# Kernel optimization log

Measured on AMD Instinct MI355X. Metric: run time of the kernel, lower is better.

The kernel has to match this reference:

```python
import jax, jax.numpy as jnp
import numpy as np

D_MODEL = 1024
NUM_ATOMS = 16384
TEMPERATURE = 1.0
NEG_INF = -1e9


def setup_inputs() -> dict:
    key = jax.random.key(0)
    kx, kd, km = jax.random.split(key, 3)
    x = jax.random.normal(kx, (4, 2048, D_MODEL), dtype=jnp.float32)
    # xavier_uniform for [num_atoms, d_model]
    limit = float(np.sqrt(6.0 / (NUM_ATOMS + D_MODEL)))
    dictionary = jax.random.uniform(
        kd, (NUM_ATOMS, D_MODEL), dtype=jnp.float32, minval=-limit, maxval=limit
    )
    mask = jax.random.randint(km, (4, 2048, NUM_ATOMS), 0, 2, dtype=jnp.int32)
    return {"x": x, "dictionary": dictionary, "mask": mask}


def reference(x, dictionary, mask):
    # scores: [b, s, num_atoms]
    scores = jnp.einsum("bsd,ad->bsa", x, dictionary)
    m = mask.astype(scores.dtype)
    scores = scores * m + (1.0 - m) * NEG_INF
    weights = jax.nn.softmax(scores / TEMPERATURE, axis=-1)
    reconstruction = jnp.einsum("bsa,ad->bsd", weights, dictionary)
    argmax_indices = jnp.argmax(scores, axis=-1)
    return reconstruction, argmax_indices
```

## Files before the change

### kernel.cpp

```cpp
#include <hip/hip_runtime.h>

#define NTOK   8192
#define DMODEL 1024
#define NATOM  16384

typedef _Float16 half8  __attribute__((ext_vector_type(8)));
typedef _Float16 half4_t __attribute__((ext_vector_type(4)));
typedef float    f32x4  __attribute__((ext_vector_type(4)));

#define GLOAD_LDS16(gsrc, ldst) \
  __builtin_amdgcn_global_load_lds((const __attribute__((address_space(1))) unsigned int*)(gsrc), \
                                   (__attribute__((address_space(3))) unsigned int*)(ldst), 16, 0, 0)

__global__ void cvt_f32_f16(const float* __restrict__ in, _Float16* __restrict__ out, int n4) {
  int i = blockIdx.x * 256 + threadIdx.x;
  if (i >= n4) return;
  float4 v = ((const float4*)in)[i];
  half4_t h;
  h[0] = (_Float16)v.x; h[1] = (_Float16)v.y; h[2] = (_Float16)v.z; h[3] = (_Float16)v.w;
  ((half4_t*)out)[i] = h;
}

__global__ void transpose_dict(const float* __restrict__ dict,
                               _Float16* __restrict__ Dh, _Float16* __restrict__ dT) {
  __shared__ _Float16 tile[64][68];
  int a0 = blockIdx.x * 64;
  int d0 = blockIdx.y * 64;
  int tid = threadIdx.x;
  int c = tid & 63;
  int r0 = tid >> 6;
  #pragma unroll
  for (int i = 0; i < 16; i++) {
    int r = r0 + i * 4;
    _Float16 h = (_Float16)dict[(size_t)(a0 + r) * DMODEL + d0 + c];
    tile[r][c] = h;
    Dh[(size_t)(a0 + r) * DMODEL + d0 + c] = h;
  }
  __syncthreads();
  #pragma unroll
  for (int i = 0; i < 16; i++) {
    int rd = r0 + i * 4;
    dT[(size_t)(d0 + rd) * NATOM + a0 + c] = tile[c][rd];
  }
}

__global__ void zero_lsum(float* __restrict__ lsum) {
  lsum[blockIdx.x * 256 + threadIdx.x] = 0.0f;
}

__device__ __forceinline__ void stage_ab(const _Float16* __restrict__ A,
                                         const _Float16* __restrict__ B,
                                         _Float16* As, _Float16* Bs,
                                         size_t arow0, size_t brow0, size_t ldk,
                                         int k0, int tid) {
  #pragma unroll
  for (int i = 0; i < 2; i++) {
    int L = tid + i * 256;
    int r = L >> 2, pc = L & 3;
    int c = pc ^ ((r >> 1) & 3);
    GLOAD_LDS16(A + (arow0 + r) * ldk + k0 + c * 8, As + (size_t)L * 8);
    GLOAD_LDS16(B + (brow0 + r) * ldk + k0 + c * 8, Bs + (size_t)L * 8);
  }
}

__launch_bounds__(256, 2)
__global__ void score_kernel(const _Float16* __restrict__ Xh,
                             const _Float16* __restrict__ Dh,
                             const int* __restrict__ mask,
                             _Float16* __restrict__ E,
                             float* __restrict__ lsum,
                             _Float16* __restrict__ Tmax) {
  __shared__ _Float16 lds[17408];
  const int tid  = threadIdx.x;
  const int lane = tid & 63;
  const int wave = tid >> 6;
  const int wm = wave >> 1, wn = wave & 1;
  const int m0 = blockIdx.y * 128;
  const int n0 = blockIdx.x * 128;

  const int frow = lane & 15;
  const int fkc  = lane >> 4;

  f32x4 acc[4][4] = {};

  stage_ab(Xh, Dh, lds, lds + 4096, m0, n0, DMODEL, 0, tid);
  int cur = 0;
  for (int it = 0; it < DMODEL / 32; ++it) {
    __syncthreads();
    if (it + 1 < DMODEL / 32)
      stage_ab(Xh, Dh, lds + (cur ^ 1) * 8192, lds + (cur ^ 1) * 8192 + 4096,
               m0, n0, DMODEL, (it + 1) * 32, tid);
    _Float16* As = lds + cur * 8192;
    _Float16* Bs = As + 4096;
    half8 af[4], bf[4];
    #pragma unroll
    for (int i = 0; i < 4; i++) {
      int ar = wm * 64 + i * 16 + frow;
      int br = wn * 64 + i * 16 + frow;
      af[i] = *(const half8*)&As[ar * 32 + (fkc ^ ((ar >> 1) & 3)) * 8];
      bf[i] = *(const half8*)&Bs[br * 32 + (fkc ^ ((br >> 1) & 3)) * 8];
    }
    #pragma unroll
    for (int i = 0; i < 4; i++)
      #pragma unroll
      for (int j = 0; j < 4; j++)
        acc[i][j] = __builtin_amdgcn_mfma_f32_16x16x32_f16(af[i], bf[j], acc[i][j], 0, 0, 0);
    cur ^= 1;
  }

  __syncthreads();
  const int cr = (lane >> 4) * 4;
  const int cc = lane & 15;
  #pragma unroll
  for (int i = 0; i < 4; i++) {
    #pragma unroll
    for (int j = 0; j < 4; j++) {
      #pragma unroll
      for (int r = 0; r < 4; r++) {
        int lr = wm * 64 + i * 16 + cr + r;
        int lc = wn * 64 + j * 16 + cc;
        int mk = mask[(size_t)(m0 + lr) * NATOM + (n0 + lc)];
        float e = mk ? __expf(acc[i][j][r]) : 0.0f;
        lds[lr * 136 + lc] = (_Float16)e;
      }
    }
  }
  __syncthreads();
  #pragma unroll
  for (int i = 0; i < 8; i++) {
    int chunk = i * 256 + tid;
    int r  = chunk >> 4;
    int c8 = (chunk & 15) * 8;
    *(half8*)&E[(size_t)(m0 + r) * NATOM + n0 + c8] = *(const half8*)&lds[r * 136 + c8];
  }
  {
    int r = tid >> 1, h = tid & 1;
    const _Float16* rowp = &lds[r * 136 + h * 64];
    float s = 0.0f, m = 0.0f;
    #pragma unroll
    for (int i = 0; i < 8; i++) {
      half8 v = *(const half8*)&rowp[i * 8];
      #pragma unroll
      for (int j = 0; j < 8; j++) { float f = (float)v[j]; s += f; m = fmaxf(m, f); }
    }
    s += __shfl_xor(s, 1, 64);
    m = fmaxf(m, __shfl_xor(m, 1, 64));
    if (h == 0) {
      atomicAdd(&lsum[m0 + r], s);
      Tmax[(size_t)blockIdx.x * NTOK + m0 + r] = (_Float16)m;
    }
  }
}

__global__ void scan_lite(const _Float16* __restrict__ E,
                          const _Float16* __restrict__ Tmax,
                          const float* __restrict__ x,
                          const float* __restrict__ dict,
                          float* __restrict__ argout) {
  const int t = blockIdx.x;
  const int lane = threadIdx.x;
  float m0 = (float)Tmax[(size_t)lane * NTOK + t];
  float m1 = (float)Tmax[(size_t)(64 + lane) * NTOK + t];
  float mx = fmaxf(m0, m1);
  #pragma unroll
  for (int off = 32; off > 0; off >>= 1) mx = fmaxf(mx, __shfl_xor(mx, off, 64));

  __shared__ int cnt;
  __shared__ int cand[32];
  __shared__ double csc[32];
  if (lane == 0) cnt = 0;
  __syncthreads();

  if (mx > 0.0f) {
    float thr = 0.98f * mx;
    unsigned long long q0 = __ballot(m0 >= thr);
    unsigned long long q1 = __ballot(m1 >= thr);
    while (q0 | q1) {
      int tile;
      if (q0) { tile = __ffsll(q0) - 1; q0 &= q0 - 1; }
      else    { tile = 64 + __ffsll(q1) - 1; q1 &= q1 - 1; }
      const _Float16* ep = E + (size_t)t * NATOM + tile * 128;
      float e0 = (float)ep[lane], e1 = (float)ep[64 + lane];
      if (e0 >= thr) { int p = atomicAdd(&cnt, 1); if (p < 32) cand[p] = tile * 128 + lane; }
      if (e1 >= thr) { int p = atomicAdd(&cnt, 1); if (p < 32) cand[p] = tile * 128 + 64 + lane; }
    }
  }
  __syncthreads();
  int nc = min(cnt, 32);
  const float* xr = x + (size_t)t * DMODEL;
  for (int c = 0; c < nc; c++) {
    const float* dr = dict + (size_t)cand[c] * DMODEL;
    double a = 0.0;
    #pragma unroll
    for (int i = 0; i < 16; i++) {
      int d = lane + i * 64;
      a += (double)xr[d] * (double)dr[d];
    }
    #pragma unroll
    for (int off = 32; off > 0; off >>= 1) a += __shfl_down(a, off, 64);
    if (lane == 0) csc[c] = a;
  }
  __syncthreads();
  if (lane == 0) {
    int best = 0;
    if (nc > 0) {
      double bs = -1e300;
      best = NATOM;
      for (int c = 0; c < nc; c++)
        if (csc[c] > bs || (csc[c] == bs && cand[c] < best)) { bs = csc[c]; best = cand[c]; }
    }
    argout[t] = (float)best;
  }
}

__launch_bounds__(256, 2)
__global__ void recon_kernel(const _Float16* __restrict__ E,
                             const _Float16* __restrict__ DT,
                             const float* __restrict__ lsum,
                             float* __restrict__ out) {
  __shared__ _Float16 lds[20480];
  const int tid  = threadIdx.x;
  const int lane = tid & 63;
  const int wave = tid >> 6;
  const int m0 = blockIdx.y * 64;
  const int n0 = blockIdx.x * 256;

  const int frow = lane & 15;
  const int fkc  = lane >> 4;

  f32x4 acc[4][4] = {};

  auto stage = [&](int k0, int b) {
    _Float16* As = lds + b * 10240;
    _Float16* Bs = As + 2048;
    {
      int L = tid;
      int r = L >> 2, pc = L & 3;
      int c = pc ^ ((r >> 1) & 3);
      GLOAD_LDS16(E + (size_t)(m0 + r) * NATOM + k0 + c * 8, As + (size_t)L * 8);
    }
    #pragma unroll
    for (int i = 0; i < 4; i++) {
      int L = tid + i * 256;
      int r = L >> 2, pc = L & 3;
      int c = pc ^ ((r >> 1) & 3);
      GLOAD_LDS16(DT + (size_t)(n0 + r) * NATOM + k0 + c * 8, Bs + (size_t)L * 8);
    }
  };

  stage(0, 0);
  int cur = 0;
  for (int it = 0; it < NATOM / 32; ++it) {
    __syncthreads();
    if (it + 1 < NATOM / 32) stage((it + 1) * 32, cur ^ 1);
    _Float16* As = lds + cur * 10240;
    _Float16* Bs = As + 2048;
    half8 af[4], bf[4];
    #pragma unroll
    for (int i = 0; i < 4; i++) {
      int ar = i * 16 + frow;
      int br = wave * 64 + i * 16 + frow;
      af[i] = *(const half8*)&As[ar * 32 + (fkc ^ ((ar >> 1) & 3)) * 8];
      bf[i] = *(const half8*)&Bs[br * 32 + (fkc ^ ((br >> 1) & 3)) * 8];
    }
    #pragma unroll
    for (int i = 0; i < 4; i++)
      #pragma unroll
      for (int j = 0; j < 4; j++)
        acc[i][j] = __builtin_amdgcn_mfma_f32_16x16x32_f16(af[i], bf[j], acc[i][j], 0, 0, 0);
    cur ^= 1;
  }

  const int cr = (lane >> 4) * 4;
  const int cc = lane & 15;
  #pragma unroll
  for (int i = 0; i < 4; i++) {
    #pragma unroll
    for (int r = 0; r < 4; r++) {
      int lr = i * 16 + cr + r;
      float sc = 1.0f / lsum[m0 + lr];
      #pragma unroll
      for (int j = 0; j < 4; j++) {
        int lc = wave * 64 + j * 16 + cc;
        out[(size_t)(m0 + lr) * DMODEL + (n0 + lc)] = acc[i][j][r] * sc;
      }
    }
  }
}

extern "C" void kernel_launch(void* const* d_in, const int* in_sizes, int n_in,
                              void* d_out, int out_size, void* d_ws, size_t ws_size,
                              hipStream_t stream) {
  const float* x    = (const float*)d_in[0];
  const float* dict = (const float*)d_in[1];
  const int*   mask = (const int*)d_in[2];
  float* recon  = (float*)d_out;
  float* argout = recon + (size_t)NTOK * DMODEL;

  char* w = (char*)d_ws;
  _Float16* Xh = (_Float16*)(w);
  _Float16* Dh = (_Float16*)(w + (size_t)16  * 1024 * 1024);
  _Float16* DT = (_Float16*)(w + (size_t)48  * 1024 * 1024);
  _Float16* E  = (_Float16*)(w + (size_t)80  * 1024 * 1024);
  float*  lsum = (float*)  (w + (size_t)336 * 1024 * 1024);
  _Float16* Tmax = (_Float16*)d_out;

  cvt_f32_f16<<<dim3(NTOK * DMODEL / 4 / 256), 256, 0, stream>>>(x, Xh, NTOK * DMODEL / 4);
  transpose_dict<<<dim3(NATOM / 64, DMODEL / 64), 256, 0, stream>>>(dict, Dh, DT);
  zero_lsum<<<dim3(NTOK / 256), 256, 0, stream>>>(lsum);
  score_kernel<<<dim3(NATOM / 128, NTOK / 128), 256, 0, stream>>>(Xh, Dh, mask, E, lsum, Tmax);
  scan_lite<<<dim3(NTOK), 64, 0, stream>>>(E, Tmax, x, dict, argout);
  recon_kernel<<<dim3(DMODEL / 256, NTOK / 64), 256, 0, stream>>>(E, DT, lsum, recon);
}
```

Measured before the change: 1.503 ms.

## Deepen GEMM pipelines to four LDS stages and swizzle block order

Both GEMM kernels move from double-buffered LDS staging to a 4-buffer ring with three tiles prefetched ahead. Explicit vmcnt waits and raw barriers replace __syncthreads, and s_setprio raises wave priority around the MFMA block. Block indices are remapped to a 1D grid with an XCD-style swizzle so neighbouring tiles share L2. The recon kernel changes its tile from 64x256 to 128x128 with a 2x2 wave layout. The aim is to hide global-load latency and improve cache reuse, at the cost of more LDS per block, which may reduce occupancy.

```diff
diff --git a/kernel.cpp b/kernel.cpp
--- a/kernel.cpp
+++ b/kernel.cpp
@@ -70,42 +70,53 @@
                              _Float16* __restrict__ E,
                              float* __restrict__ lsum,
                              _Float16* __restrict__ Tmax) {
-  __shared__ _Float16 lds[17408];
+  __shared__ _Float16 lds[32768];
   const int tid  = threadIdx.x;
   const int lane = tid & 63;
   const int wave = tid >> 6;
   const int wm = wave >> 1, wn = wave & 1;
-  const int m0 = blockIdx.y * 128;
-  const int n0 = blockIdx.x * 128;
+  const int swz = (blockIdx.x & 7) * 1024 + (blockIdx.x >> 3);
+  const int nt = swz & 127;
+  const int n0 = nt * 128;
+  const int m0 = (swz >> 7) * 128;
 
   const int frow = lane & 15;
   const int fkc  = lane >> 4;
 
   f32x4 acc[4][4] = {};
 
-  stage_ab(Xh, Dh, lds, lds + 4096, m0, n0, DMODEL, 0, tid);
-  int cur = 0;
-  for (int it = 0; it < DMODEL / 32; ++it) {
-    __syncthreads();
-    if (it + 1 < DMODEL / 32)
-      stage_ab(Xh, Dh, lds + (cur ^ 1) * 8192, lds + (cur ^ 1) * 8192 + 4096,
-               m0, n0, DMODEL, (it + 1) * 32, tid);
-    _Float16* As = lds + cur * 8192;
-    _Float16* Bs = As + 4096;
+  stage_ab(Xh, Dh, lds,         lds + 4096,  m0, n0, DMODEL, 0,  tid);
+  stage_ab(Xh, Dh, lds + 8192,  lds + 12288, m0, n0, DMODEL, 32, tid);
+  stage_ab(Xh, Dh, lds + 16384, lds + 20480, m0, n0, DMODEL, 64, tid);
+
+  for (int t = 0; t < 32; ++t) {
+    if (t < 30)       asm volatile("s_waitcnt vmcnt(8)" ::: "memory");
+    else if (t == 30) asm volatile("s_waitcnt vmcnt(4)" ::: "memory");
+    else              asm volatile("s_waitcnt vmcnt(0)" ::: "memory");
+    __builtin_amdgcn_s_barrier();
+    __builtin_amdgcn_sched_barrier(0);
+    const _Float16* As = lds + (t & 3) * 8192;
+    const _Float16* Bs = As + 4096;
     half8 af[4], bf[4];
     #pragma unroll
     for (int i = 0; i < 4; i++) {
       int ar = wm * 64 + i * 16 + frow;
       int br = wn * 64 + i * 16 + frow;
-      af[i] = *(const half8*)&As[ar * 32 + (fkc ^ ((ar >> 1) & 3)) * 8];
-      bf[i] = *(const half8*)&Bs[br * 32 + (fkc ^ ((br >> 1) & 3)) * 8];
-    }
+      af[i] = *(const half8*)&As[ar * 32 + ((fkc ^ ((ar >> 1) & 3)) << 3)];
+      bf[i] = *(const half8*)&Bs[br * 32 + ((fkc ^ ((br >> 1) & 3)) << 3)];
+    }
+    if (t + 3 < 32) {
+      int b = (t + 3) & 3;
+      stage_ab(Xh, Dh, lds + b * 8192, lds + b * 8192 + 4096, m0, n0, DMODEL, (t + 3) * 32, tid);
+    }
+    __builtin_amdgcn_s_setprio(1);
     #pragma unroll
     for (int i = 0; i < 4; i++)
       #pragma unroll
       for (int j = 0; j < 4; j++)
         acc[i][j] = __builtin_amdgcn_mfma_f32_16x16x32_f16(af[i], bf[j], acc[i][j], 0, 0, 0);
-    cur ^= 1;
+    __builtin_amdgcn_s_setprio(0);
+    __builtin_amdgcn_sched_barrier(0);
   }
 
   __syncthreads();
@@ -147,7 +158,7 @@
     m = fmaxf(m, __shfl_xor(m, 1, 64));
     if (h == 0) {
       atomicAdd(&lsum[m0 + r], s);
-      Tmax[(size_t)blockIdx.x * NTOK + m0 + r] = (_Float16)m;
+      Tmax[(size_t)nt * NTOK + m0 + r] = (_Float16)m;
     }
   }
 }
@@ -218,57 +229,52 @@
                              const _Float16* __restrict__ DT,
                              const float* __restrict__ lsum,
                              float* __restrict__ out) {
-  __shared__ _Float16 lds[20480];
+  __shared__ _Float16 lds[32768];
   const int tid  = threadIdx.x;
   const int lane = tid & 63;
   const int wave = tid >> 6;
-  const int m0 = blockIdx.y * 64;
-  const int n0 = blockIdx.x * 256;
+  const int wm = wave >> 1, wn = wave & 1;
+  const int swz = (blockIdx.x & 7) * 64 + (blockIdx.x >> 3);
+  const int n0 = (swz & 7) * 128;
+  const int m0 = (swz >> 3) * 128;
 
   const int frow = lane & 15;
   const int fkc  = lane >> 4;
 
   f32x4 acc[4][4] = {};
 
-  auto stage = [&](int k0, int b) {
-    _Float16* As = lds + b * 10240;
-    _Float16* Bs = As + 2048;
-    {
-      int L = tid;
-      int r = L >> 2, pc = L & 3;
-      int c = pc ^ ((r >> 1) & 3);
-      GLOAD_LDS16(E + (size_t)(m0 + r) * NATOM + k0 + c * 8, As + (size_t)L * 8);
-    }
+  stage_ab(E, DT, lds,         lds + 4096,  m0, n0, NATOM, 0,  tid);
+  stage_ab(E, DT, lds + 8192,  lds + 12288, m0, n0, NATOM, 32, tid);
+  stage_ab(E, DT, lds + 16384, lds + 20480, m0, n0, NATOM, 64, tid);
+
+  for (int t = 0; t < 512; ++t) {
+    if (t < 510)       asm volatile("s_waitcnt vmcnt(8)" ::: "memory");
+    else if (t == 510) asm volatile("s_waitcnt vmcnt(4)" ::: "memory");
+    else               asm volatile("s_waitcnt vmcnt(0)" ::: "memory");
+    __builtin_amdgcn_s_barrier();
+    __builtin_amdgcn_sched_barrier(0);
+    const _Float16* As = lds + (t & 3) * 8192;
+    const _Float16* Bs = As + 4096;
+    half8 af[4], bf[4];
     #pragma unroll
     for (int i = 0; i < 4; i++) {
-      int L = tid + i * 256;
-      int r = L >> 2, pc = L & 3;
-      int c = pc ^ ((r >> 1) & 3);
-      GLOAD_LDS16(DT + (size_t)(n0 + r) * NATOM + k0 + c * 8, Bs + (size_t)L * 8);
-    }
-  };
-
-  stage(0, 0);
-  int cur = 0;
-  for (int it = 0; it < NATOM / 32; ++it) {
-    __syncthreads();
-    if (it + 1 < NATOM / 32) stage((it + 1) * 32, cur ^ 1);
-    _Float16* As = lds + cur * 10240;
-    _Float16* Bs = As + 2048;
-    half8 af[4], bf[4];
-    #pragma unroll
-    for (int i = 0; i < 4; i++) {
-      int ar = i * 16 + frow;
-      int br = wave * 64 + i * 16 + frow;
-      af[i] = *(const half8*)&As[ar * 32 + (fkc ^ ((ar >> 1) & 3)) * 8];
-      bf[i] = *(const half8*)&Bs[br * 32 + (fkc ^ ((br >> 1) & 3)) * 8];
-    }
+      int ar = wm * 64 + i * 16 + frow;
+      int br = wn * 64 + i * 16 + frow;
+      af[i] = *(const half8*)&As[ar * 32 + ((fkc ^ ((ar >> 1) & 3)) << 3)];
+      bf[i] = *(const half8*)&Bs[br * 32 + ((fkc ^ ((br >> 1) & 3)) << 3)];
+    }
+    if (t + 3 < 512) {
+      int b = (t + 3) & 3;
+      stage_ab(E, DT, lds + b * 8192, lds + b * 8192 + 4096, m0, n0, NATOM, (t + 3) * 32, tid);
+    }
+    __builtin_amdgcn_s_setprio(1);
     #pragma unroll
     for (int i = 0; i < 4; i++)
       #pragma unroll
       for (int j = 0; j < 4; j++)
         acc[i][j] = __builtin_amdgcn_mfma_f32_16x16x32_f16(af[i], bf[j], acc[i][j], 0, 0, 0);
-    cur ^= 1;
+    __builtin_amdgcn_s_setprio(0);
+    __builtin_amdgcn_sched_barrier(0);
   }
 
   const int cr = (lane >> 4) * 4;
@@ -277,11 +283,11 @@
   for (int i = 0; i < 4; i++) {
     #pragma unroll
     for (int r = 0; r < 4; r++) {
-      int lr = i * 16 + cr + r;
+      int lr = wm * 64 + i * 16 + cr + r;
       float sc = 1.0f / lsum[m0 + lr];
       #pragma unroll
       for (int j = 0; j < 4; j++) {
-        int lc = wave * 64 + j * 16 + cc;
+        int lc = wn * 64 + j * 16 + cc;
         out[(size_t)(m0 + lr) * DMODEL + (n0 + lc)] = acc[i][j][r] * sc;
       }
     }
@@ -308,7 +314,7 @@
   cvt_f32_f16<<<dim3(NTOK * DMODEL / 4 / 256), 256, 0, stream>>>(x, Xh, NTOK * DMODEL / 4);
   transpose_dict<<<dim3(NATOM / 64, DMODEL / 64), 256, 0, stream>>>(dict, Dh, DT);
   zero_lsum<<<dim3(NTOK / 256), 256, 0, stream>>>(lsum);
-  score_kernel<<<dim3(NATOM / 128, NTOK / 128), 256, 0, stream>>>(Xh, Dh, mask, E, lsum, Tmax);
+  score_kernel<<<dim3(8192), 256, 0, stream>>>(Xh, Dh, mask, E, lsum, Tmax);
   scan_lite<<<dim3(NTOK), 64, 0, stream>>>(E, Tmax, x, dict, argout);
-  recon_kernel<<<dim3(DMODEL / 256, NTOK / 64), 256, 0, stream>>>(E, DT, lsum, recon);
-}
+  recon_kernel<<<dim3(512), 256, 0, stream>>>(E, DT, lsum, recon);
+}
```

New measurement: 1.439 ms. 1.04x faster.

## Triple-buffer GEMM pipelines with vmcnt waits and retile recon for XCD locality

Applied to the files above, without the earlier changes.

Both the score and recon GEMM main loops move from double-buffered staging with __syncthreads to a three-stage LDS ring. Each loop waits on a partial vmcnt, then raises wave priority around the MFMAs so global loads stay in flight longer. The recon kernel switches to 64x128 tiles with a 2x2 wave layout and a 1D grid that groups M tiles per XCD for better cache reuse. Launch bounds rise to target higher occupancy. The trade-offs are more register and LDS pressure in score and less reuse per recon block.

```diff
diff --git a/kernel.cpp b/kernel.cpp
--- a/kernel.cpp
+++ b/kernel.cpp
@@ -63,14 +63,14 @@
   }
 }
 
-__launch_bounds__(256, 2)
+__launch_bounds__(256, 3)
 __global__ void score_kernel(const _Float16* __restrict__ Xh,
                              const _Float16* __restrict__ Dh,
                              const int* __restrict__ mask,
                              _Float16* __restrict__ E,
                              float* __restrict__ lsum,
                              _Float16* __restrict__ Tmax) {
-  __shared__ _Float16 lds[17408];
+  __shared__ _Float16 lds[24576];
   const int tid  = threadIdx.x;
   const int lane = tid & 63;
   const int wave = tid >> 6;
@@ -83,29 +83,37 @@
 
   f32x4 acc[4][4] = {};
 
-  stage_ab(Xh, Dh, lds, lds + 4096, m0, n0, DMODEL, 0, tid);
-  int cur = 0;
-  for (int it = 0; it < DMODEL / 32; ++it) {
-    __syncthreads();
-    if (it + 1 < DMODEL / 32)
-      stage_ab(Xh, Dh, lds + (cur ^ 1) * 8192, lds + (cur ^ 1) * 8192 + 4096,
-               m0, n0, DMODEL, (it + 1) * 32, tid);
-    _Float16* As = lds + cur * 8192;
-    _Float16* Bs = As + 4096;
+  stage_ab(Xh, Dh, lds,        lds + 4096,  m0, n0, DMODEL, 0,  tid);
+  stage_ab(Xh, Dh, lds + 8192, lds + 12288, m0, n0, DMODEL, 32, tid);
+
+  for (int t = 0; t < 32; ++t) {
+    if (t < 31) asm volatile("s_waitcnt vmcnt(4)" ::: "memory");
+    else        asm volatile("s_waitcnt vmcnt(0)" ::: "memory");
+    __builtin_amdgcn_s_barrier();
+    __builtin_amdgcn_sched_barrier(0);
+    const int b = t % 3;
+    const _Float16* As = lds + b * 8192;
+    const _Float16* Bs = As + 4096;
     half8 af[4], bf[4];
     #pragma unroll
     for (int i = 0; i < 4; i++) {
       int ar = wm * 64 + i * 16 + frow;
       int br = wn * 64 + i * 16 + frow;
-      af[i] = *(const half8*)&As[ar * 32 + (fkc ^ ((ar >> 1) & 3)) * 8];
-      bf[i] = *(const half8*)&Bs[br * 32 + (fkc ^ ((br >> 1) & 3)) * 8];
-    }
+      af[i] = *(const half8*)&As[ar * 32 + ((fkc ^ ((ar >> 1) & 3)) << 3)];
+      bf[i] = *(const half8*)&Bs[br * 32 + ((fkc ^ ((br >> 1) & 3)) << 3)];
+    }
+    if (t + 2 < 32) {
+      int nb = (t + 2) % 3;
+      stage_ab(Xh, Dh, lds + nb * 8192, lds + nb * 8192 + 4096, m0, n0, DMODEL, (t + 2) * 32, tid);
+    }
+    __builtin_amdgcn_s_setprio(1);
     #pragma unroll
     for (int i = 0; i < 4; i++)
       #pragma unroll
       for (int j = 0; j < 4; j++)
         acc[i][j] = __builtin_amdgcn_mfma_f32_16x16x32_f16(af[i], bf[j], acc[i][j], 0, 0, 0);
-    cur ^= 1;
+    __builtin_amdgcn_s_setprio(0);
+    __builtin_amdgcn_sched_barrier(0);
   }
 
   __syncthreads();
@@ -213,25 +221,31 @@
   }
 }
 
-__launch_bounds__(256, 2)
+__launch_bounds__(256, 4)
 __global__ void recon_kernel(const _Float16* __restrict__ E,
                              const _Float16* __restrict__ DT,
                              const float* __restrict__ lsum,
                              float* __restrict__ out) {
-  __shared__ _Float16 lds[20480];
+  __shared__ _Float16 lds[18432];
   const int tid  = threadIdx.x;
   const int lane = tid & 63;
   const int wave = tid >> 6;
-  const int m0 = blockIdx.y * 64;
-  const int n0 = blockIdx.x * 256;
+  const int wm = wave >> 1, wn = wave & 1;
+  const int bid = blockIdx.x;
+  const int xcd = bid & 7;
+  const int idx = bid >> 3;
+  const int mt  = xcd * 16 + (idx & 15);
+  const int nt  = idx >> 4;
+  const int m0 = mt * 64;
+  const int n0 = nt * 128;
 
   const int frow = lane & 15;
   const int fkc  = lane >> 4;
 
-  f32x4 acc[4][4] = {};
+  f32x4 acc[2][4] = {};
 
   auto stage = [&](int k0, int b) {
-    _Float16* As = lds + b * 10240;
+    _Float16* As = lds + b * 6144;
     _Float16* Bs = As + 2048;
     {
       int L = tid;
@@ -240,7 +254,7 @@
       GLOAD_LDS16(E + (size_t)(m0 + r) * NATOM + k0 + c * 8, As + (size_t)L * 8);
     }
     #pragma unroll
-    for (int i = 0; i < 4; i++) {
+    for (int i = 0; i < 2; i++) {
       int L = tid + i * 256;
       int r = L >> 2, pc = L & 3;
       int c = pc ^ ((r >> 1) & 3);
@@ -249,39 +263,49 @@
   };
 
   stage(0, 0);
-  int cur = 0;
-  for (int it = 0; it < NATOM / 32; ++it) {
-    __syncthreads();
-    if (it + 1 < NATOM / 32) stage((it + 1) * 32, cur ^ 1);
-    _Float16* As = lds + cur * 10240;
-    _Float16* Bs = As + 2048;
-    half8 af[4], bf[4];
-    #pragma unroll
-    for (int i = 0; i < 4; i++) {
-      int ar = i * 16 + frow;
-      int br = wave * 64 + i * 16 + frow;
-      af[i] = *(const half8*)&As[ar * 32 + (fkc ^ ((ar >> 1) & 3)) * 8];
-      bf[i] = *(const half8*)&Bs[br * 32 + (fkc ^ ((br >> 1) & 3)) * 8];
-    }
-    #pragma unroll
-    for (int i = 0; i < 4; i++)
+  stage(32, 1);
+
+  for (int t = 0; t < 512; ++t) {
+    if (t < 511) asm volatile("s_waitcnt vmcnt(3)" ::: "memory");
+    else         asm volatile("s_waitcnt vmcnt(0)" ::: "memory");
+    __builtin_amdgcn_s_barrier();
+    __builtin_amdgcn_sched_barrier(0);
+    const int b = t % 3;
+    const _Float16* As = lds + b * 6144;
+    const _Float16* Bs = As + 2048;
+    half8 af[2], bf[4];
+    #pragma unroll
+    for (int i = 0; i < 2; i++) {
+      int ar = wm * 32 + i * 16 + frow;
+      af[i] = *(const half8*)&As[ar * 32 + ((fkc ^ ((ar >> 1) & 3)) << 3)];
+    }
+    #pragma unroll
+    for (int j = 0; j < 4; j++) {
+      int br = wn * 64 + j * 16 + frow;
+      bf[j] = *(const half8*)&Bs[br * 32 + ((fkc ^ ((br >> 1) & 3)) << 3)];
+    }
+    if (t + 2 < 512) stage((t + 2) * 32, (t + 2) % 3);
+    __builtin_amdgcn_s_setprio(1);
+    #pragma unroll
+    for (int i = 0; i < 2; i++)
       #pragma unroll
       for (int j = 0; j < 4; j++)
         acc[i][j] = __builtin_amdgcn_mfma_f32_16x16x32_f16(af[i], bf[j], acc[i][j], 0, 0, 0);
-    cur ^= 1;
+    __builtin_amdgcn_s_setprio(0);
+    __builtin_amdgcn_sched_barrier(0);
   }
 
   const int cr = (lane >> 4) * 4;
   const int cc = lane & 15;
   #pragma unroll
-  for (int i = 0; i < 4; i++) {
+  for (int i = 0; i < 2; i++) {
     #pragma unroll
     for (int r = 0; r < 4; r++) {
-      int lr = i * 16 + cr + r;
+      int lr = wm * 32 + i * 16 + cr + r;
       float sc = 1.0f / lsum[m0 + lr];
       #pragma unroll
       for (int j = 0; j < 4; j++) {
-        int lc = wave * 64 + j * 16 + cc;
+        int lc = wn * 64 + j * 16 + cc;
         out[(size_t)(m0 + lr) * DMODEL + (n0 + lc)] = acc[i][j][r] * sc;
       }
     }
@@ -310,5 +334,5 @@
   zero_lsum<<<dim3(NTOK / 256), 256, 0, stream>>>(lsum);
   score_kernel<<<dim3(NATOM / 128, NTOK / 128), 256, 0, stream>>>(Xh, Dh, mask, E, lsum, Tmax);
   scan_lite<<<dim3(NTOK), 64, 0, stream>>>(E, Tmax, x, dict, argout);
-  recon_kernel<<<dim3(DMODEL / 256, NTOK / 64), 256, 0, stream>>>(E, DT, lsum, recon);
-}
+  recon_kernel<<<dim3(1024), 256, 0, stream>>>(E, DT, lsum, recon);
+}
```

Result: no change. 1.524 ms (+1.4%).
